# Kernel optimization log

Measured on AMD Instinct MI355X. Metric: run time of the kernel, lower is better.

## Reference

```python
import jax, jax.numpy as jnp
import numpy as np

D = 768  # n_dim


def setup_inputs() -> dict:
    key = jax.random.key(0)
    ks = jax.random.split(key, 9)
    B, S = 4, 4096
    s = 0.02
    return {
        "x": jax.random.normal(ks[0], (B, S, D), dtype=jnp.float32),
        "Wq": jax.random.normal(ks[1], (D, D), dtype=jnp.float32) * s,
        "bq": jax.random.normal(ks[2], (D,), dtype=jnp.float32) * s,
        "Wk": jax.random.normal(ks[3], (D, D), dtype=jnp.float32) * s,
        "bk": jax.random.normal(ks[4], (D,), dtype=jnp.float32) * s,
        "Wv": jax.random.normal(ks[5], (D, D), dtype=jnp.float32) * s,
        "bv": jax.random.normal(ks[6], (D,), dtype=jnp.float32) * s,
        "Wc": jax.random.normal(ks[7], (D, D), dtype=jnp.float32) * s,
        "bc": jax.random.normal(ks[8], (D,), dtype=jnp.float32) * s,
    }


def reference(x, Wq, bq, Wk, bk, Wv, bv, Wc, bc):
    # Faithful to the source's executed math (its head-reshape and masked_fill
    # results are discarded): single-'head' full-dim attention, NO causal mask,
    # scale = n_dim**-0.5, then a transpose(1,2).reshape element permutation.
    B, S, nd = x.shape
    q = jnp.einsum('bsd,ed->bse', x, Wq) + bq  # nn.Linear: x @ W.T + b
    k = jnp.einsum('bsd,ed->bse', x, Wk) + bk
    v = jnp.einsum('bsd,ed->bse', x, Wv) + bv
    att = jnp.einsum('bqd,bkd->bqk', q, k) * (nd ** -0.5)  # [B,S,S]
    att = jax.nn.softmax(att, axis=-1)  # no mask (bug preserved)
    y = jnp.einsum('bqk,bkd->bqd', att, v)  # [B,S,D]
    y = jnp.transpose(y, (0, 2, 1)).reshape(B, S, nd)  # element permutation (bug preserved)
    return jnp.einsum('bsd,ed->bse', y, Wc) + bc
```

## Files before the change

### kernel.cpp

```cpp
#include <hip/hip_runtime.h>
#include <stdint.h>


typedef __bf16 bf16;
typedef __bf16 bf16x4 __attribute__((ext_vector_type(4)));
typedef __bf16 bf16x8 __attribute__((ext_vector_type(8)));
typedef float f32x4 __attribute__((ext_vector_type(4)));

#define OFF_Q    0L
#define OFF_K    25165824L
#define OFF_VT   50331648L
#define OFF_W    75497472L
#define OFF_B    80216064L
#define OFF_FLAG 80222208L
#define OFF_ATT  80223232L
#define ATT_B    33554432L
#define SD       3145728L

__device__ __forceinline__ void glds16(const void* g, void* s) {
  __builtin_amdgcn_global_load_lds((const __attribute__((address_space(1))) void*)g,
                                   (__attribute__((address_space(3))) void*)s, 16, 0, 0);
}

__global__ void sniff_dtype(const uint16_t* __restrict__ x, int* __restrict__ flag)
{
  const int t = threadIdx.x;
  int bad = 0;
  for (int i = t; i < 4096; i += 256) {
    const int e = (x[2 * i] >> 7) & 0xFF;
    bad |= (e >= 0xE0);
  }
  __shared__ int s;
  if (t == 0) s = 0;
  __syncthreads();
  if (bad) s = 1;
  __syncthreads();
  if (t == 0) *flag = s;
}

__global__ void normalize8(const void* __restrict__ src, bf16* __restrict__ dst,
                           long n8, const int* __restrict__ flag)
{
  const long i = (long)blockIdx.x * 256 + threadIdx.x;
  if (i >= n8) return;
  bf16x8 o;
  if (*flag) {
    const float4 a = ((const float4*)src)[2 * i];
    const float4 b = ((const float4*)src)[2 * i + 1];
    o[0] = (bf16)a.x; o[1] = (bf16)a.y; o[2] = (bf16)a.z; o[3] = (bf16)a.w;
    o[4] = (bf16)b.x; o[5] = (bf16)b.y; o[6] = (bf16)b.z; o[7] = (bf16)b.w;
  } else {
    o = ((const bf16x8*)src)[i];
  }
  ((bf16x8*)dst)[i] = o;
}

__launch_bounds__(256, 2)
__global__ void gemm_bt(const bf16* __restrict__ A, int lda, long strideA,
                        const bf16* __restrict__ Bm, int ldb, long strideB,
                        void* __restrict__ Cv, int ldc, long strideC,
                        int K, const bf16* __restrict__ bias, float alpha,
                        int transC, const int* __restrict__ oflag)
{
  __shared__ bf16 As[128 * 32];
  __shared__ bf16 Bs[128 * 32];
  A  += (long)blockIdx.z * strideA;
  Bm += (long)blockIdx.z * strideB;
  const int outf32 = (oflag != nullptr) && (*oflag != 0);
  const int tid = threadIdx.x;
  const int wave = tid >> 6, lane = tid & 63;
  const int lr = lane & 15, quad = lane >> 4;
  const int wm = (wave >> 1) * 64, wn = (wave & 1) * 64;
  const long m0 = (long)blockIdx.y * 128, n0 = (long)blockIdx.x * 128;

  f32x4 acc[4][4];
  const f32x4 zero = {0.f, 0.f, 0.f, 0.f};
#pragma unroll
  for (int i = 0; i < 4; ++i)
#pragma unroll
    for (int j = 0; j < 4; ++j) acc[i][j] = zero;

  const int r0 = tid >> 2, c0 = (tid & 3) * 8;
  const bf16* pA0 = A + (m0 + r0) * (long)lda + c0;
  const bf16* pA1 = A + (m0 + 64 + r0) * (long)lda + c0;
  const bf16* pB0 = Bm + (n0 + r0) * (long)ldb + c0;
  const bf16* pB1 = Bm + (n0 + 64 + r0) * (long)ldb + c0;
  bf16* sA0 = As + wave * 512;
  bf16* sA1 = As + 2048 + wave * 512;
  bf16* sB0 = Bs + wave * 512;
  bf16* sB1 = Bs + 2048 + wave * 512;

  for (int k0 = 0; k0 < K; k0 += 32) {
    __syncthreads();
    glds16(pA0 + k0, sA0);
    glds16(pA1 + k0, sA1);
    glds16(pB0 + k0, sB0);
    glds16(pB1 + k0, sB1);
    __syncthreads();
    bf16x8 aF[4], bF[4];
#pragma unroll
    for (int i = 0; i < 4; ++i) {
      aF[i] = *(const bf16x8*)(As + (wm + i * 16 + lr) * 32 + quad * 8);
      bF[i] = *(const bf16x8*)(Bs + (wn + i * 16 + lr) * 32 + quad * 8);
    }
#pragma unroll
    for (int i = 0; i < 4; ++i)
#pragma unroll
      for (int j = 0; j < 4; ++j)
        acc[i][j] = __builtin_amdgcn_mfma_f32_16x16x32_bf16(aF[i], bF[j], acc[i][j], 0, 0, 0);
  }

#pragma unroll
  for (int j = 0; j < 4; ++j) {
    const long col = n0 + wn + j * 16 + lr;
    const float bv = bias ? (float)bias[col] : 0.f;
#pragma unroll
    for (int i = 0; i < 4; ++i) {
      const long row = m0 + wm + i * 16 + quad * 4;
      if (transC) {
        bf16x4 v4;
#pragma unroll
        for (int r = 0; r < 4; ++r) v4[r] = (bf16)((acc[i][j][r] + bv) * alpha);
        *(bf16x4*)((bf16*)Cv + (long)blockIdx.z * strideC + col * (long)ldc + row) = v4;
      } else if (outf32) {
#pragma unroll
        for (int r = 0; r < 4; ++r)
          ((float*)Cv)[(long)blockIdx.z * strideC + (row + r) * (long)ldc + col] =
              (acc[i][j][r] + bv) * alpha;
      } else {
#pragma unroll
        for (int r = 0; r < 4; ++r)
          ((bf16*)Cv)[(long)blockIdx.z * strideC + (row + r) * (long)ldc + col] =
              (bf16)((acc[i][j][r] + bv) * alpha);
      }
    }
  }
}

__launch_bounds__(256)
__global__ void softmax_rows(bf16* __restrict__ att)
{
  bf16* p = att + (size_t)blockIdx.x * 4096;
  const int t = threadIdx.x;
  bf16x8 v0 = *(const bf16x8*)(p + t * 16);
  bf16x8 v1 = *(const bf16x8*)(p + t * 16 + 8);
  float x[16];
#pragma unroll
  for (int i = 0; i < 8; ++i) { x[i] = (float)v0[i]; x[8 + i] = (float)v1[i]; }
  float m = x[0];
#pragma unroll
  for (int i = 1; i < 16; ++i) m = fmaxf(m, x[i]);
#pragma unroll
  for (int off = 32; off > 0; off >>= 1) m = fmaxf(m, __shfl_down(m, off));
  __shared__ float redm[4], reds[4];
  if ((t & 63) == 0) redm[t >> 6] = m;
  __syncthreads();
  m = fmaxf(fmaxf(redm[0], redm[1]), fmaxf(redm[2], redm[3]));
  float s = 0.f;
#pragma unroll
  for (int i = 0; i < 16; ++i) { x[i] = __expf(x[i] - m); s += x[i]; }
#pragma unroll
  for (int off = 32; off > 0; off >>= 1) s += __shfl_down(s, off);
  if ((t & 63) == 0) reds[t >> 6] = s;
  __syncthreads();
  s = reds[0] + reds[1] + reds[2] + reds[3];
  const float inv = 1.f / s;
#pragma unroll
  for (int i = 0; i < 8; ++i) { v0[i] = (bf16)(x[i] * inv); v1[i] = (bf16)(x[8 + i] * inv); }
  *(bf16x8*)(p + t * 16) = v0;
  *(bf16x8*)(p + t * 16 + 8) = v1;
}

extern "C" void kernel_launch(void* const* d_in, const int* in_sizes, int n_in,
                              void* d_out, int out_size, void* d_ws, size_t ws_size,
                              hipStream_t stream)
{
  (void)in_sizes; (void)n_in; (void)out_size;
  char* ws = (char*)d_ws;

  if (ws_size < (size_t)(OFF_ATT + ATT_B)) return;
  const size_t avail = ws_size - (size_t)OFF_ATT;
  int group = (int)(avail / (size_t)ATT_B);
  group = group >= 4 ? 4 : (group >= 2 ? 2 : 1);

  bf16* q   = (bf16*)(ws + OFF_Q);
  bf16* k   = (bf16*)(ws + OFF_K);
  bf16* vT2 = (bf16*)(ws + OFF_VT);
  bf16* Wn  = (bf16*)(ws + OFF_W);
  bf16* bn  = (bf16*)(ws + OFF_B);
  int*  flg = (int*)(ws + OFF_FLAG);
  bf16* att = (bf16*)(ws + OFF_ATT);
  bf16* xn  = att;

  dim3 blk(256, 1, 1);
  const float qs = 0.03608439182435161f;

  sniff_dtype<<<1, blk, 0, stream>>>((const uint16_t*)d_in[0], flg);
  normalize8<<<6144, blk, 0, stream>>>(d_in[0], xn, 1572864L, flg);
  for (int w = 0; w < 4; ++w) {
    normalize8<<<288, blk, 0, stream>>>(d_in[1 + 2 * w], Wn + w * 589824L, 73728L, flg);
    normalize8<<<1, blk, 0, stream>>>(d_in[2 + 2 * w], bn + w * 768L, 96L, flg);
  }

  dim3 gproj(6, 128, 1);
  gemm_bt<<<gproj, blk, 0, stream>>>(xn, 768, 0, Wn + 0 * 589824L, 768, 0,
                                     q, 768, 0, 768, bn + 0, qs, 0, nullptr);
  gemm_bt<<<gproj, blk, 0, stream>>>(xn, 768, 0, Wn + 1 * 589824L, 768, 0,
                                     k, 768, 0, 768, bn + 768, 1.f, 0, nullptr);
  gemm_bt<<<gproj, blk, 0, stream>>>(xn, 768, 0, Wn + 2 * 589824L, 768, 0,
                                     vT2, 16384, 0, 768, bn + 1536, 1.f, 1, nullptr);

  for (int g = 0; g < 4; g += group) {
    dim3 gs(32, 32, group);
    gemm_bt<<<gs, blk, 0, stream>>>(q + g * SD, 768, SD, k + g * SD, 768, SD,
                                    att, 4096, 16777216L, 768, nullptr, 1.f, 0, nullptr);
    softmax_rows<<<group * 4096, blk, 0, stream>>>(att);
    dim3 gpv(32, 6, group);
    gemm_bt<<<gpv, blk, 0, stream>>>(vT2 + g * 4096L, 16384, 4096L,
                                     att, 4096, 16777216L,
                                     q + g * SD, 4096, SD, 4096, nullptr, 1.f, 0, nullptr);
  }

  dim3 gout(6, 128, 1);
  gemm_bt<<<gout, blk, 0, stream>>>(q, 768, 0, Wn + 3 * 589824L, 768, 0,
                                    d_out, 768, 0, 768, bn + 2304, 1.f, 0, flg);
}
```

Baseline: 565.0 us.

## Fuse softmax into QK and PV GEMM epilogues via exp-sum atomics

Removes the separate softmax pass. The QK^T GEMM epilogue now writes exp(scores) and atomically accumulates row sums into a float buffer, and the PV GEMM epilogue divides by those sums. The MFMA operand order is also swapped for the non-transposed modes so each lane owns four consecutive columns, which allows vectorised bf16x4/f32x4 stores. The max subtraction is dropped, so very large scores could overflow exp; it adds atomics and a zeroing kernel.

```diff
diff --git a/kernel.cpp b/kernel.cpp
--- a/kernel.cpp
+++ b/kernel.cpp
@@ -13,9 +13,15 @@
 #define OFF_W    75497472L
 #define OFF_B    80216064L
 #define OFF_FLAG 80222208L
-#define OFF_ATT  80223232L
+#define OFF_L    80223232L
+#define OFF_ATT  80289792L
 #define ATT_B    33554432L
 #define SD       3145728L
+
+#define M_PLAIN  0
+#define M_TRANSC 1
+#define M_EXPSUM 2
+#define M_DIVL   3
 
 __device__ __forceinline__ void glds16(const void* g, void* s) {
   __builtin_amdgcn_global_load_lds((const __attribute__((address_space(1))) void*)g,
@@ -55,18 +61,24 @@
   ((bf16x8*)dst)[i] = o;
 }
 
+__global__ void zero_f32(float* __restrict__ p)
+{
+  p[(long)blockIdx.x * 256 + threadIdx.x] = 0.f;
+}
+
 __launch_bounds__(256, 2)
 __global__ void gemm_bt(const bf16* __restrict__ A, int lda, long strideA,
                         const bf16* __restrict__ Bm, int ldb, long strideB,
                         void* __restrict__ Cv, int ldc, long strideC,
                         int K, const bf16* __restrict__ bias, float alpha,
-                        int transC, const int* __restrict__ oflag)
+                        int mode, const int* __restrict__ oflag,
+                        float* __restrict__ lsum)
 {
   __shared__ bf16 As[128 * 32];
   __shared__ bf16 Bs[128 * 32];
   A  += (long)blockIdx.z * strideA;
   Bm += (long)blockIdx.z * strideB;
-  const int outf32 = (oflag != nullptr) && (*oflag != 0);
+  if (lsum) lsum += (long)blockIdx.z * 4096L;
   const int tid = threadIdx.x;
   const int wave = tid >> 6, lane = tid & 63;
   const int lr = lane & 15, quad = lane >> 4;
@@ -103,72 +115,89 @@
       aF[i] = *(const bf16x8*)(As + (wm + i * 16 + lr) * 32 + quad * 8);
       bF[i] = *(const bf16x8*)(Bs + (wn + i * 16 + lr) * 32 + quad * 8);
     }
-#pragma unroll
-    for (int i = 0; i < 4; ++i)
-#pragma unroll
-      for (int j = 0; j < 4; ++j)
-        acc[i][j] = __builtin_amdgcn_mfma_f32_16x16x32_bf16(aF[i], bF[j], acc[i][j], 0, 0, 0);
-  }
-
-#pragma unroll
-  for (int j = 0; j < 4; ++j) {
-    const long col = n0 + wn + j * 16 + lr;
-    const float bv = bias ? (float)bias[col] : 0.f;
-#pragma unroll
-    for (int i = 0; i < 4; ++i) {
-      const long row = m0 + wm + i * 16 + quad * 4;
-      if (transC) {
+    if (mode == M_TRANSC) {
+#pragma unroll
+      for (int i = 0; i < 4; ++i)
+#pragma unroll
+        for (int j = 0; j < 4; ++j)
+          acc[i][j] = __builtin_amdgcn_mfma_f32_16x16x32_bf16(aF[i], bF[j], acc[i][j], 0, 0, 0);
+    } else {
+#pragma unroll
+      for (int i = 0; i < 4; ++i)
+#pragma unroll
+        for (int j = 0; j < 4; ++j)
+          acc[i][j] = __builtin_amdgcn_mfma_f32_16x16x32_bf16(bF[j], aF[i], acc[i][j], 0, 0, 0);
+    }
+  }
+
+  if (mode == M_TRANSC) {
+#pragma unroll
+    for (int j = 0; j < 4; ++j) {
+      const long col = n0 + wn + j * 16 + lr;
+      const float bv = bias ? (float)bias[col] : 0.f;
+#pragma unroll
+      for (int i = 0; i < 4; ++i) {
+        const long row = m0 + wm + i * 16 + quad * 4;
         bf16x4 v4;
 #pragma unroll
         for (int r = 0; r < 4; ++r) v4[r] = (bf16)((acc[i][j][r] + bv) * alpha);
         *(bf16x4*)((bf16*)Cv + (long)blockIdx.z * strideC + col * (long)ldc + row) = v4;
-      } else if (outf32) {
-#pragma unroll
-        for (int r = 0; r < 4; ++r)
-          ((float*)Cv)[(long)blockIdx.z * strideC + (row + r) * (long)ldc + col] =
-              (acc[i][j][r] + bv) * alpha;
+      }
+    }
+    return;
+  }
+
+  const int outf32 = (oflag != nullptr) && (*oflag != 0);
+  long colb[4];
+  f32x4 addv[4];
+#pragma unroll
+  for (int j = 0; j < 4; ++j) {
+    colb[j] = n0 + wn + j * 16 + quad * 4;
+    if (mode == M_PLAIN) {
+      const bf16x4 bb = *(const bf16x4*)(bias + colb[j]);
+#pragma unroll
+      for (int r = 0; r < 4; ++r) addv[j][r] = (float)bb[r];
+    } else if (mode == M_DIVL) {
+      const f32x4 lv = *(const f32x4*)(lsum + colb[j]);
+#pragma unroll
+      for (int r = 0; r < 4; ++r) addv[j][r] = 1.0f / lv[r];
+    }
+  }
+#pragma unroll
+  for (int i = 0; i < 4; ++i) {
+    const long row = m0 + wm + i * 16 + lr;
+    char* rowp = (char*)Cv + ((long)blockIdx.z * strideC + row * (long)ldc) * (outf32 ? 4 : 2);
+    float rsum = 0.f;
+#pragma unroll
+    for (int j = 0; j < 4; ++j) {
+      f32x4 v;
+#pragma unroll
+      for (int r = 0; r < 4; ++r) {
+        float t = acc[i][j][r];
+        if (mode == M_PLAIN)       t = (t + addv[j][r]) * alpha;
+        else if (mode == M_EXPSUM) t = __expf(t);
+        else if (mode == M_DIVL)   t = t * addv[j][r];
+        v[r] = t;
+      }
+      if (outf32) {
+        *(f32x4*)(rowp + colb[j] * 4) = v;
       } else {
-#pragma unroll
-        for (int r = 0; r < 4; ++r)
-          ((bf16*)Cv)[(long)blockIdx.z * strideC + (row + r) * (long)ldc + col] =
-              (bf16)((acc[i][j][r] + bv) * alpha);
+        bf16x4 v4;
+#pragma unroll
+        for (int r = 0; r < 4; ++r) v4[r] = (bf16)v[r];
+        if (mode == M_EXPSUM) {
+#pragma unroll
+          for (int r = 0; r < 4; ++r) rsum += (float)v4[r];
+        }
+        *(bf16x4*)(rowp + colb[j] * 2) = v4;
       }
     }
-  }
-}
-
-__launch_bounds__(256)
-__global__ void softmax_rows(bf16* __restrict__ att)
-{
-  bf16* p = att + (size_t)blockIdx.x * 4096;
-  const int t = threadIdx.x;
-  bf16x8 v0 = *(const bf16x8*)(p + t * 16);
-  bf16x8 v1 = *(const bf16x8*)(p + t * 16 + 8);
-  float x[16];
-#pragma unroll
-  for (int i = 0; i < 8; ++i) { x[i] = (float)v0[i]; x[8 + i] = (float)v1[i]; }
-  float m = x[0];
-#pragma unroll
-  for (int i = 1; i < 16; ++i) m = fmaxf(m, x[i]);
-#pragma unroll
-  for (int off = 32; off > 0; off >>= 1) m = fmaxf(m, __shfl_down(m, off));
-  __shared__ float redm[4], reds[4];
-  if ((t & 63) == 0) redm[t >> 6] = m;
-  __syncthreads();
-  m = fmaxf(fmaxf(redm[0], redm[1]), fmaxf(redm[2], redm[3]));
-  float s = 0.f;
-#pragma unroll
-  for (int i = 0; i < 16; ++i) { x[i] = __expf(x[i] - m); s += x[i]; }
-#pragma unroll
-  for (int off = 32; off > 0; off >>= 1) s += __shfl_down(s, off);
-  if ((t & 63) == 0) reds[t >> 6] = s;
-  __syncthreads();
-  s = reds[0] + reds[1] + reds[2] + reds[3];
-  const float inv = 1.f / s;
-#pragma unroll
-  for (int i = 0; i < 8; ++i) { v0[i] = (bf16)(x[i] * inv); v1[i] = (bf16)(x[8 + i] * inv); }
-  *(bf16x8*)(p + t * 16) = v0;
-  *(bf16x8*)(p + t * 16 + 8) = v1;
+    if (mode == M_EXPSUM) {
+      rsum += __shfl_xor(rsum, 16);
+      rsum += __shfl_xor(rsum, 32);
+      if (quad == 0) atomicAdd(&lsum[row], rsum);
+    }
+  }
 }
 
 extern "C" void kernel_launch(void* const* d_in, const int* in_sizes, int n_in,
@@ -183,14 +212,15 @@
   int group = (int)(avail / (size_t)ATT_B);
   group = group >= 4 ? 4 : (group >= 2 ? 2 : 1);
 
-  bf16* q   = (bf16*)(ws + OFF_Q);
-  bf16* k   = (bf16*)(ws + OFF_K);
-  bf16* vT2 = (bf16*)(ws + OFF_VT);
-  bf16* Wn  = (bf16*)(ws + OFF_W);
-  bf16* bn  = (bf16*)(ws + OFF_B);
-  int*  flg = (int*)(ws + OFF_FLAG);
-  bf16* att = (bf16*)(ws + OFF_ATT);
-  bf16* xn  = att;
+  bf16*  q    = (bf16*)(ws + OFF_Q);
+  bf16*  k    = (bf16*)(ws + OFF_K);
+  bf16*  vT2  = (bf16*)(ws + OFF_VT);
+  bf16*  Wn   = (bf16*)(ws + OFF_W);
+  bf16*  bn   = (bf16*)(ws + OFF_B);
+  int*   flg  = (int*)(ws + OFF_FLAG);
+  float* lbase= (float*)(ws + OFF_L);
+  bf16*  att  = (bf16*)(ws + OFF_ATT);
+  bf16*  xn   = att;
 
   dim3 blk(256, 1, 1);
   const float qs = 0.03608439182435161f;
@@ -201,27 +231,29 @@
     normalize8<<<288, blk, 0, stream>>>(d_in[1 + 2 * w], Wn + w * 589824L, 73728L, flg);
     normalize8<<<1, blk, 0, stream>>>(d_in[2 + 2 * w], bn + w * 768L, 96L, flg);
   }
+  zero_f32<<<64, blk, 0, stream>>>(lbase);
 
   dim3 gproj(6, 128, 1);
   gemm_bt<<<gproj, blk, 0, stream>>>(xn, 768, 0, Wn + 0 * 589824L, 768, 0,
-                                     q, 768, 0, 768, bn + 0, qs, 0, nullptr);
+                                     q, 768, 0, 768, bn + 0, qs, M_PLAIN, nullptr, nullptr);
   gemm_bt<<<gproj, blk, 0, stream>>>(xn, 768, 0, Wn + 1 * 589824L, 768, 0,
-                                     k, 768, 0, 768, bn + 768, 1.f, 0, nullptr);
+                                     k, 768, 0, 768, bn + 768, 1.f, M_PLAIN, nullptr, nullptr);
   gemm_bt<<<gproj, blk, 0, stream>>>(xn, 768, 0, Wn + 2 * 589824L, 768, 0,
-                                     vT2, 16384, 0, 768, bn + 1536, 1.f, 1, nullptr);
+                                     vT2, 16384, 0, 768, bn + 1536, 1.f, M_TRANSC, nullptr, nullptr);
 
   for (int g = 0; g < 4; g += group) {
     dim3 gs(32, 32, group);
     gemm_bt<<<gs, blk, 0, stream>>>(q + g * SD, 768, SD, k + g * SD, 768, SD,
-                                    att, 4096, 16777216L, 768, nullptr, 1.f, 0, nullptr);
-    softmax_rows<<<group * 4096, blk, 0, stream>>>(att);
+                                    att, 4096, 16777216L, 768, nullptr, 1.f,
+                                    M_EXPSUM, nullptr, lbase + g * 4096L);
     dim3 gpv(32, 6, group);
     gemm_bt<<<gpv, blk, 0, stream>>>(vT2 + g * 4096L, 16384, 4096L,
                                      att, 4096, 16777216L,
-                                     q + g * SD, 4096, SD, 4096, nullptr, 1.f, 0, nullptr);
+                                     q + g * SD, 4096, SD, 4096, nullptr, 1.f,
+                                     M_DIVL, nullptr, lbase + g * 4096L);
   }
 
   dim3 gout(6, 128, 1);
   gemm_bt<<<gout, blk, 0, stream>>>(q, 768, 0, Wn + 3 * 589824L, 768, 0,
-                                    d_out, 768, 0, 768, bn + 2304, 1.f, 0, flg);
-}
+                                    d_out, 768, 0, 768, bn + 2304, 1.f, M_PLAIN, flg, nullptr);
+}
```

Result: slower. 737.9 us (+30.6%).
